# Kernel tuning notes

Hardware: AMD Instinct MI355X
Metric: run time of the kernel (lower is better)

Reference implementation:

```python
import jax, jax.numpy as jnp
import numpy as np

N = 50000      # nodes
E = 1600000    # edges (avg degree 32)
F_IN = 128     # num_features
DIM = 64       # hidden dim
L = 3          # num_gc_layers
G = 500        # graphs in batch


def setup_inputs() -> dict:
    key = jax.random.key(0)
    ks = jax.random.split(key, 16)
    inp = {}
    inp["x"] = jax.random.normal(ks[0], (N, F_IN), dtype=jnp.float32)
    inp["edge_index"] = jax.random.randint(ks[1], (2, E), 0, N, dtype=jnp.int32)
    inp["batch"] = jnp.sort(jax.random.randint(ks[2], (N,), 0, G, dtype=jnp.int32))
    # GIN layer MLP params: layer0 maps F_IN->DIM->DIM, later layers DIM->DIM->DIM
    d_in = F_IN
    ki = 3
    for i in range(L):
        inp[f"W1_{i}"] = jax.random.normal(ks[ki], (d_in, DIM), dtype=jnp.float32) / np.sqrt(d_in); ki += 1
        inp[f"b1_{i}"] = jnp.zeros((DIM,), dtype=jnp.float32)
        inp[f"W2_{i}"] = jax.random.normal(ks[ki], (DIM, DIM), dtype=jnp.float32) / np.sqrt(DIM); ki += 1
        inp[f"b2_{i}"] = jnp.zeros((DIM,), dtype=jnp.float32)
        d_in = DIM
    # final scoring head: concat readout -> dim * L inputs, 1 output
    inp["Wm"] = jax.random.normal(ks[ki], (DIM * L, 1), dtype=jnp.float32) / np.sqrt(DIM * L)
    inp["bm"] = jnp.zeros((1,), dtype=jnp.float32)
    return inp


def _segment_softmax(scores, seg, num_segments):
    # numerically stable softmax over elements grouped by seg; scores [M, 1]
    m = jax.ops.segment_max(scores, seg, num_segments=num_segments)
    e = jnp.exp(scores - m[seg])
    denom = jax.ops.segment_sum(e, seg, num_segments=num_segments)
    return e / denom[seg]


def _forward(x, edge_index, batch, params):
    src, dst = edge_index[0], edge_index[1]
    n = x.shape[0]
    xs = []
    h = x
    for i in range(L):
        W1, b1, W2, b2 = params[4 * i: 4 * i + 4]
        # GINConv (eps=0): h_i <- MLP(h_i + sum_{j->i} h_j)
        agg = jax.ops.segment_sum(h[src], dst, num_segments=n)
        h = jax.nn.relu((h + agg) @ W1 + b1) @ W2 + b2
        if i != L - 1:
            h = jax.nn.relu(h)
        xs.append(h)
    node_prob = jnp.concatenate(xs, axis=1)            # concat readout [N, DIM*L]
    Wm, bm = params[4 * L], params[4 * L + 1]
    node_score = node_prob @ Wm + bm                   # [N, 1]
    # lift_node_score_to_edge_score
    src_score = node_score[src]                        # [E, 1]
    dst_score = node_score[dst]
    edge_score = src_score * dst_score
    edge_prop = _segment_softmax(edge_score, dst, n)   # softmax over edges per dst
    new_score = jax.ops.segment_sum(src_score * edge_prop, dst, num_segments=n)
    node_score = node_score + new_score
    # final softmax over nodes grouped by graph id
    return _segment_softmax(node_score, batch, G)


def reference(x, edge_index, batch, W1_0, b1_0, W2_0, b2_0, W1_1, b1_1, W2_1, b2_1,
              W1_2, b1_2, W2_2, b2_2, Wm, bm):
    params = [W1_0, b1_0, W2_0, b2_0, W1_1, b1_1, W2_1, b2_1,
              W1_2, b1_2, W2_2, b2_2, Wm, bm]
    return _forward(x, edge_index, batch, params)
```

## Files before the change

kernel.cpp:

```cpp
#include <hip/hip_runtime.h>
#include <hip/hip_fp16.h>
#include <math.h>

#define N_NODES 50000
#define N_EDGES 1600000
#define N_GRAPH 500
#define CHUNKS 128
#define EPC (N_EDGES / CHUNKS)
#define NP1 (N_NODES + 1)
#define NIT ((EPC + 1023) / 1024)
#define HALF_N (N_NODES / 2)
#define HNP1 (HALF_N + 1)

__device__ __forceinline__ float rl(float v, int k) {
    return __int_as_float(__builtin_amdgcn_readlane(__float_as_int(v), k));
}
__device__ __forceinline__ void hacc16(float4& A, float4& B, uint4 w) {
    float2 f0 = __half22float2(*reinterpret_cast<__half2*>(&w.x));
    float2 f1 = __half22float2(*reinterpret_cast<__half2*>(&w.y));
    float2 f2 = __half22float2(*reinterpret_cast<__half2*>(&w.z));
    float2 f3 = __half22float2(*reinterpret_cast<__half2*>(&w.w));
    A.x += f0.x; A.y += f0.y; A.z += f1.x; A.w += f1.y;
    B.x += f2.x; B.y += f2.y; B.z += f3.x; B.w += f3.y;
}

__global__ __launch_bounds__(1024) void histsort_kernel(const int* __restrict__ src,
                                                        const int* __restrict__ dst,
                                                        int* __restrict__ csrc_chunk,
                                                        unsigned short* __restrict__ locs) {
    __shared__ unsigned packed[HALF_N / 2];
    __shared__ unsigned aux[1024];
    const int c = blockIdx.x >> 1;
    const int h = blockIdx.x & 1;
    const int lo = h * HALF_N;
    const int s0 = c * EPC;
    const int tid = threadIdx.x;

    for (int i = tid; i < HALF_N / 2; i += 1024) packed[i] = 0;
    __syncthreads();

    unsigned short lrv[NIT];
#pragma unroll
    for (int it = 0; it < NIT; it++) {
        int e = s0 + it * 1024 + tid;
        if (e < s0 + EPC) {
            int d = dst[e];
            int ld = d - lo;
            if (ld >= 0 && ld < HALF_N) {
                int sh = (ld & 1) * 16;
                unsigned old = atomicAdd(&packed[ld >> 1], 1u << sh);
                lrv[it] = (unsigned short)((old >> sh) & 0xffffu);
            }
        }
    }
    __syncthreads();

    const int W = 13;
    int w0 = tid * W;
    int w1 = min(w0 + W, HALF_N / 2);
    unsigned run = 0;
    for (int i = w0; i < w1; i++) {
        unsigned v = packed[i];
        unsigned plo = v & 0xffffu, phi = v >> 16;
        packed[i] = run | ((run + plo) << 16);
        run += plo + phi;
    }
    aux[tid] = run;
    __syncthreads();
    for (int off = 1; off < 1024; off <<= 1) {
        unsigned t = (tid >= off) ? aux[tid - off] : 0;
        __syncthreads();
        aux[tid] += t;
        __syncthreads();
    }
    unsigned b0 = (tid == 0) ? 0 : aux[tid - 1];
    if (b0) {
        unsigned addv = b0 | (b0 << 16);
        for (int i = w0; i < w1; i++) packed[i] += addv;
    }
    __syncthreads();
    unsigned total = aux[1023];

    int* outc = csrc_chunk + (size_t)(c * 2 + h) * EPC;
#pragma unroll
    for (int it = 0; it < NIT; it++) {
        int e = s0 + it * 1024 + tid;
        if (e < s0 + EPC) {
            int d = dst[e];
            int ld = d - lo;
            if (ld >= 0 && ld < HALF_N) {
                unsigned pw = packed[ld >> 1];
                unsigned loc = (ld & 1) ? (pw >> 16) : (pw & 0xffffu);
                outc[loc + lrv[it]] = src[e];
            }
        }
    }
    unsigned short* lc = locs + (size_t)(c * 2 + h) * HNP1;
    for (int ld = tid; ld <= HALF_N; ld += 1024) {
        unsigned short v;
        if (ld == HALF_N) {
            v = (unsigned short)total;
        } else {
            unsigned pw = packed[ld >> 1];
            v = (unsigned short)((ld & 1) ? (pw >> 16) : (pw & 0xffffu));
        }
        lc[ld] = v;
    }
}

__global__ __launch_bounds__(1024) void base_scan1_kernel(const unsigned short* __restrict__ locs,
                                                          unsigned short* __restrict__ base,
                                                          int* __restrict__ deg,
                                                          int* __restrict__ part, int N) {
    int d = blockIdx.x * 1024 + threadIdx.x;
    int run = 0;
    if (d < N) {
        int h = (d >= HALF_N) ? 1 : 0;
        int ld = d - h * HALF_N;
#pragma unroll 8
        for (int c = 0; c < CHUNKS; c++) {
            const unsigned short* lc = locs + (size_t)(c * 2 + h) * HNP1;
            int l0 = lc[ld];
            int l1 = lc[ld + 1];
            base[(size_t)c * N + d] = (unsigned short)run;
            run += l1 - l0;
        }
        deg[d] = run;
    }
    int v = run;
#pragma unroll
    for (int o = 32; o >= 1; o >>= 1) v += __shfl_xor(v, o);
    __shared__ int red[16];
    if ((threadIdx.x & 63) == 0) red[threadIdx.x >> 6] = v;
    __syncthreads();
    if (threadIdx.x == 0) {
        int s = 0;
#pragma unroll
        for (int k = 0; k < 16; k++) s += red[k];
        part[blockIdx.x] = s;
    }
}

__global__ __launch_bounds__(1024) void scan3_kernel(const int* __restrict__ deg,
                                                     const int* __restrict__ part,
                                                     int* __restrict__ rowptr, int N, int nb) {
    __shared__ int blockOff;
    __shared__ int wsum[16];
    int lane = threadIdx.x & 63;
    int w = threadIdx.x >> 6;
    if (threadIdx.x < 64) {
        int pv = (lane < nb && lane < (int)blockIdx.x) ? part[lane] : 0;
#pragma unroll
        for (int o = 32; o >= 1; o >>= 1) pv += __shfl_xor(pv, o);
        if (lane == 0) blockOff = pv;
    }
    int i = blockIdx.x * 1024 + threadIdx.x;
    int v = (i < N) ? deg[i] : 0;
    int inc = v;
#pragma unroll
    for (int o = 1; o < 64; o <<= 1) {
        int t = __shfl_up(inc, o);
        if (lane >= o) inc += t;
    }
    if (lane == 63) wsum[w] = inc;
    __syncthreads();
    if (threadIdx.x < 16) {
        int x = wsum[threadIdx.x];
        int xo = x;
#pragma unroll
        for (int o = 1; o < 16; o <<= 1) {
            int t = __shfl_up(x, o);
            if ((int)threadIdx.x >= o) x += t;
        }
        wsum[threadIdx.x] = x - xo;
    }
    __syncthreads();
    int b = blockOff + wsum[w];
    if (i < N) {
        rowptr[i] = b + inc - v;
        if (i == N - 1) rowptr[N] = b + inc;
    }
}

__global__ __launch_bounds__(256) void gatherfill_kernel(const int* __restrict__ csrc_chunk,
                                                         const unsigned short* __restrict__ locs,
                                                         const unsigned short* __restrict__ base,
                                                         const int* __restrict__ rowptr,
                                                         int* __restrict__ csr_src) {
    const int perXcd = N_NODES / 8;
    int xcd = blockIdx.x & 7;
    int idx = (blockIdx.x >> 3) * 4 + (threadIdx.x >> 6);
    if (idx >= perXcd) return;
    int wid = xcd * perXcd + idx;
    int lane = threadIdx.x & 63;
    int h = (wid >= HALF_N) ? 1 : 0;
    int ld = wid - h * HALF_N;
    int rp = rowptr[wid];
#pragma unroll
    for (int cc = 0; cc < 2; cc++) {
        int c = lane + cc * 64;
        const unsigned short* lc = locs + (size_t)(c * 2 + h) * HNP1;
        int l0 = lc[ld];
        int l1 = lc[ld + 1];
        int cnt = l1 - l0;
        int ob = rp + (int)base[(size_t)c * N_NODES + wid];
        const int* in = csrc_chunk + (size_t)(c * 2 + h) * EPC + l0;
        for (int i = 0; i < cnt; i++) csr_src[ob + i] = in[i];
    }
}

__global__ __launch_bounds__(256, 2) void gemm0_kernel(const float* __restrict__ x,
                                                       const float* __restrict__ W1,
                                                       __half* __restrict__ y0,
                                                       int N, int totalWaves) {
    int lane = threadIdx.x & 63;
    int wid = (blockIdx.x * 256 + threadIdx.x) >> 6;
    float wA[64], wB[64];
#pragma unroll
    for (int k = 0; k < 64; k++) wA[k] = W1[k * 64 + lane];
#pragma unroll
    for (int k = 0; k < 64; k++) wB[k] = W1[(64 + k) * 64 + lane];
    for (int node = wid; node < N; node += totalWaves) {
        float xa = x[(size_t)node * 128 + lane];
        float xb = x[(size_t)node * 128 + 64 + lane];
        float a0 = 0.f, a1 = 0.f, a2 = 0.f, a3 = 0.f;
#pragma unroll
        for (int k = 0; k < 64; k += 4) {
            a0 = fmaf(rl(xa, k + 0), wA[k + 0], a0);
            a1 = fmaf(rl(xa, k + 1), wA[k + 1], a1);
            a2 = fmaf(rl(xa, k + 2), wA[k + 2], a2);
            a3 = fmaf(rl(xa, k + 3), wA[k + 3], a3);
        }
#pragma unroll
        for (int k = 0; k < 64; k += 4) {
            a0 = fmaf(rl(xb, k + 0), wB[k + 0], a0);
            a1 = fmaf(rl(xb, k + 1), wB[k + 1], a1);
            a2 = fmaf(rl(xb, k + 2), wB[k + 2], a2);
            a3 = fmaf(rl(xb, k + 3), wB[k + 3], a3);
        }
        y0[(size_t)node * 64 + lane] = __float2half((a0 + a1) + (a2 + a3));
    }
}

__global__ __launch_bounds__(256) void agg_kernel(const __half* __restrict__ yh,
                                                  const int* __restrict__ rowptr,
                                                  const int* __restrict__ csr_src,
                                                  float* __restrict__ u, int N) {
    int wv = (blockIdx.x * 256 + threadIdx.x) >> 6;
    int half = (threadIdx.x >> 5) & 1;
    int node = wv * 2 + half;
    if (node >= N) return;
    int lane = threadIdx.x & 31;
    int q = lane >> 3;
    int r = lane & 7;
    int start = rowptr[node];
    int end = rowptr[node + 1];
    float4 A = make_float4(0.f, 0.f, 0.f, 0.f);
    float4 B = make_float4(0.f, 0.f, 0.f, 0.f);
    int j = start;
    for (; j + 32 <= end; j += 32) {
        int s0 = csr_src[j + q];
        int s1 = csr_src[j + 4 + q];
        int s2 = csr_src[j + 8 + q];
        int s3 = csr_src[j + 12 + q];
        int s4 = csr_src[j + 16 + q];
        int s5 = csr_src[j + 20 + q];
        int s6 = csr_src[j + 24 + q];
        int s7 = csr_src[j + 28 + q];
        uint4 w0 = *(const uint4*)(yh + (size_t)s0 * 64 + r * 8);
        uint4 w1 = *(const uint4*)(yh + (size_t)s1 * 64 + r * 8);
        uint4 w2 = *(const uint4*)(yh + (size_t)s2 * 64 + r * 8);
        uint4 w3 = *(const uint4*)(yh + (size_t)s3 * 64 + r * 8);
        uint4 w4 = *(const uint4*)(yh + (size_t)s4 * 64 + r * 8);
        uint4 w5 = *(const uint4*)(yh + (size_t)s5 * 64 + r * 8);
        uint4 w6 = *(const uint4*)(yh + (size_t)s6 * 64 + r * 8);
        uint4 w7 = *(const uint4*)(yh + (size_t)s7 * 64 + r * 8);
        hacc16(A, B, w0); hacc16(A, B, w1); hacc16(A, B, w2); hacc16(A, B, w3);
        hacc16(A, B, w4); hacc16(A, B, w5); hacc16(A, B, w6); hacc16(A, B, w7);
    }
#pragma unroll
    for (int m = 0; m < 8; m++) {
        int e = j + 4 * m + q;
        if (e < end) {
            int s = csr_src[e];
            uint4 w = *(const uint4*)(yh + (size_t)s * 64 + r * 8);
            hacc16(A, B, w);
        }
    }
#pragma unroll
    for (int o = 8; o <= 16; o <<= 1) {
        A.x += __shfl_xor(A.x, o); A.y += __shfl_xor(A.y, o);
        A.z += __shfl_xor(A.z, o); A.w += __shfl_xor(A.w, o);
        B.x += __shfl_xor(B.x, o); B.y += __shfl_xor(B.y, o);
        B.z += __shfl_xor(B.z, o); B.w += __shfl_xor(B.w, o);
    }
    if (lane < 8) {
        uint4 w = *(const uint4*)(yh + (size_t)node * 64 + r * 8);
        hacc16(A, B, w);
        *(float4*)(u + (size_t)node * 64 + r * 8) = A;
        *(float4*)(u + (size_t)node * 64 + r * 8 + 4) = B;
    }
}

template <int LAYER>
__global__ __launch_bounds__(256, 2) void mlpAB_kernel(const float* __restrict__ u,
                                                       const float* __restrict__ b1,
                                                       const float* __restrict__ W2,
                                                       const float* __restrict__ b2,
                                                       const float* __restrict__ W1n,
                                                       const float* __restrict__ Wm,
                                                       __half* __restrict__ ynext,
                                                       float* __restrict__ score,
                                                       int N, int totalWaves) {
    int lane = threadIdx.x & 63;
    int wid = (blockIdx.x * 256 + threadIdx.x) >> 6;
    float w2[64], w1[64];
#pragma unroll
    for (int k = 0; k < 64; k++) w2[k] = W2[k * 64 + lane];
#pragma unroll
    for (int k = 0; k < 64; k++) w1[k] = W1n[k * 64 + lane];
    float bb1 = b1[lane], bb2 = b2[lane], wm = Wm[LAYER * 64 + lane];

    int node = wid;
    float uin = (node < N) ? u[(size_t)node * 64 + lane] : 0.f;
    for (; node < N; node += totalWaves) {
        int nn = node + totalWaves;
        float unext = (nn < N) ? u[(size_t)nn * 64 + lane] : 0.f;
        float t = fmaxf(uin + bb1, 0.f);
        float a0 = 0.f, a1 = 0.f, a2 = 0.f, a3 = 0.f;
#pragma unroll
        for (int k = 0; k < 64; k += 4) {
            a0 = fmaf(rl(t, k + 0), w2[k + 0], a0);
            a1 = fmaf(rl(t, k + 1), w2[k + 1], a1);
            a2 = fmaf(rl(t, k + 2), w2[k + 2], a2);
            a3 = fmaf(rl(t, k + 3), w2[k + 3], a3);
        }
        float h = fmaxf(bb2 + ((a0 + a1) + (a2 + a3)), 0.f);
        float p = h * wm;
#pragma unroll
        for (int o = 32; o >= 1; o >>= 1) p += __shfl_xor(p, o);
        if (lane == 0) {
            if (LAYER == 0) score[node] = p;
            else score[node] += p;
        }
        float y0 = 0.f, y1 = 0.f, y2 = 0.f, y3 = 0.f;
#pragma unroll
        for (int k = 0; k < 64; k += 4) {
            y0 = fmaf(rl(h, k + 0), w1[k + 0], y0);
            y1 = fmaf(rl(h, k + 1), w1[k + 1], y1);
            y2 = fmaf(rl(h, k + 2), w1[k + 2], y2);
            y3 = fmaf(rl(h, k + 3), w1[k + 3], y3);
        }
        ynext[(size_t)node * 64 + lane] = __float2half((y0 + y1) + (y2 + y3));
        uin = unext;
    }
}

__global__ __launch_bounds__(256, 2) void mlpA2_kernel(const float* __restrict__ u,
                                                       const float* __restrict__ b1,
                                                       const float* __restrict__ W2,
                                                       const float* __restrict__ b2,
                                                       const float* __restrict__ Wm,
                                                       float* __restrict__ score,
                                                       int N, int totalWaves) {
    int lane = threadIdx.x & 63;
    int wid = (blockIdx.x * 256 + threadIdx.x) >> 6;
    float w2[64];
#pragma unroll
    for (int k = 0; k < 64; k++) w2[k] = W2[k * 64 + lane];
    float bb1 = b1[lane], bb2 = b2[lane], wm = Wm[2 * 64 + lane];

    int node = wid;
    float uin = (node < N) ? u[(size_t)node * 64 + lane] : 0.f;
    for (; node < N; node += totalWaves) {
        int nn = node + totalWaves;
        float unext = (nn < N) ? u[(size_t)nn * 64 + lane] : 0.f;
        float t = fmaxf(uin + bb1, 0.f);
        float a0 = 0.f, a1 = 0.f, a2 = 0.f, a3 = 0.f;
#pragma unroll
        for (int k = 0; k < 64; k += 4) {
            a0 = fmaf(rl(t, k + 0), w2[k + 0], a0);
            a1 = fmaf(rl(t, k + 1), w2[k + 1], a1);
            a2 = fmaf(rl(t, k + 2), w2[k + 2], a2);
            a3 = fmaf(rl(t, k + 3), w2[k + 3], a3);
        }
        float h = bb2 + ((a0 + a1) + (a2 + a3));
        float p = h * wm;
#pragma unroll
        for (int o = 32; o >= 1; o >>= 1) p += __shfl_xor(p, o);
        if (lane == 0) score[node] += p;
        uin = unext;
    }
}

__global__ __launch_bounds__(256) void edge_softmax_kernel(const float* __restrict__ score,
                                                           const int* __restrict__ rowptr,
                                                           const int* __restrict__ csr_src,
                                                           const float* __restrict__ bm,
                                                           float* __restrict__ nsf, int N) {
    int wid = (blockIdx.x * blockDim.x + threadIdx.x) >> 6;
    int lane = threadIdx.x & 63;
    if (wid >= N) return;
    float b = bm[0];
    float sd = score[wid] + b;
    int start = rowptr[wid];
    int end = rowptr[wid + 1];
    bool has0 = (start + lane < end);
    float ss0 = 0.f;
    float m = -INFINITY;
    if (has0) {
        ss0 = score[csr_src[start + lane]] + b;
        m = ss0 * sd;
    }
    for (int j = start + 64 + lane; j < end; j += 64) {
        float ss = score[csr_src[j]] + b;
        m = fmaxf(m, ss * sd);
    }
#pragma unroll
    for (int o = 32; o >= 1; o >>= 1) m = fmaxf(m, __shfl_xor(m, o));
    float se = 0.f, swe = 0.f;
    if (m > -INFINITY) {
        if (has0) {
            float e0 = expf(ss0 * sd - m);
            se += e0;
            swe += ss0 * e0;
        }
        for (int j = start + 64 + lane; j < end; j += 64) {
            float ss = score[csr_src[j]] + b;
            float e = expf(ss * sd - m);
            se += e;
            swe += ss * e;
        }
#pragma unroll
        for (int o = 32; o >= 1; o >>= 1) {
            se += __shfl_xor(se, o);
            swe += __shfl_xor(swe, o);
        }
    }
    float ns = (se > 0.f) ? (swe / se) : 0.f;
    if (lane == 0) nsf[wid] = sd + ns;
}

__global__ __launch_bounds__(256) void graph_softmax_kernel(const float* __restrict__ nsf,
                                                            const int* __restrict__ batch,
                                                            float* __restrict__ out, int N) {
    int g = blockIdx.x;
    int tid = threadIdx.x;
    int lo = 0, hi = N;
    while (lo < hi) { int mid = (lo + hi) >> 1; if (batch[mid] < g) lo = mid + 1; else hi = mid; }
    int s0 = lo;
    hi = N;
    while (lo < hi) { int mid = (lo + hi) >> 1; if (batch[mid] < g + 1) lo = mid + 1; else hi = mid; }
    int s1 = lo;

    __shared__ float red[4];
    __shared__ float bval;
    float m = -INFINITY;
    for (int i = s0 + tid; i < s1; i += 256) m = fmaxf(m, nsf[i]);
#pragma unroll
    for (int o = 32; o >= 1; o >>= 1) m = fmaxf(m, __shfl_xor(m, o));
    if ((tid & 63) == 0) red[tid >> 6] = m;
    __syncthreads();
    if (tid == 0) bval = fmaxf(fmaxf(red[0], red[1]), fmaxf(red[2], red[3]));
    __syncthreads();
    float bmx = bval;
    float s = 0.f;
    for (int i = s0 + tid; i < s1; i += 256) {
        float e = expf(nsf[i] - bmx);
        out[i] = e;
        s += e;
    }
#pragma unroll
    for (int o = 32; o >= 1; o >>= 1) s += __shfl_xor(s, o);
    __syncthreads();
    if ((tid & 63) == 0) red[tid >> 6] = s;
    __syncthreads();
    if (tid == 0) bval = red[0] + red[1] + red[2] + red[3];
    __syncthreads();
    float inv = 1.f / bval;
    for (int i = s0 + tid; i < s1; i += 256) out[i] *= inv;
}

extern "C" void kernel_launch(void* const* d_in, const int* in_sizes, int n_in,
                              void* d_out, int out_size, void* d_ws, size_t ws_size,
                              hipStream_t stream) {
    const int N = N_NODES, E = N_EDGES;

    const float* x = (const float*)d_in[0];
    const int* ei = (const int*)d_in[1];
    const int* batch = (const int*)d_in[2];
    const float* W1a[3] = {(const float*)d_in[3], (const float*)d_in[7], (const float*)d_in[11]};
    const float* b1a[3] = {(const float*)d_in[4], (const float*)d_in[8], (const float*)d_in[12]};
    const float* W2a[3] = {(const float*)d_in[5], (const float*)d_in[9], (const float*)d_in[13]};
    const float* b2a[3] = {(const float*)d_in[6], (const float*)d_in[10], (const float*)d_in[14]};
    const float* Wm = (const float*)d_in[15];
    const float* bm = (const float*)d_in[16];
    float* out = (float*)d_out;

    const int* srcp = ei;
    const int* dstp = ei + E;

    float* ubuf = (float*)d_ws;
    int* csrc_chunk = (int*)ubuf;
    __half* yA = (__half*)(ubuf + (size_t)N * 64);
    __half* yB = yA + (size_t)N * 64;
    float* score = (float*)(yB + (size_t)N * 64);
    float* nsf = score + N;
    int* deg = (int*)(nsf + N);
    int* rowptr = deg + N;
    int* part = rowptr + N + 1;
    int* csr_src = part + 64;
    unsigned short* locs = (unsigned short*)(csr_src + E);
    unsigned short* base = locs + (size_t)2 * CHUNKS * HNP1;

    histsort_kernel<<<CHUNKS * 2, 1024, 0, stream>>>(srcp, dstp, csrc_chunk, locs);

    const int nbScan = (N + 1023) / 1024;
    base_scan1_kernel<<<nbScan, 1024, 0, stream>>>(locs, base, deg, part, N);
    scan3_kernel<<<nbScan, 1024, 0, stream>>>(deg, part, rowptr, N, nbScan);

    const int gfBlocks = 8 * ((N / 8 + 3) / 4);
    gatherfill_kernel<<<gfBlocks, 256, 0, stream>>>(csrc_chunk, locs, base, rowptr, csr_src);

    const int gw = 4096;
    gemm0_kernel<<<1024, 256, 0, stream>>>(x, W1a[0], yA, N, gw);

    int aggBlocks = (N / 2 + 3) / 4;

    agg_kernel<<<aggBlocks, 256, 0, stream>>>(yA, rowptr, csr_src, ubuf, N);
    mlpAB_kernel<0><<<1024, 256, 0, stream>>>(ubuf, b1a[0], W2a[0], b2a[0], W1a[1], Wm, yB, score, N, gw);

    agg_kernel<<<aggBlocks, 256, 0, stream>>>(yB, rowptr, csr_src, ubuf, N);
    mlpAB_kernel<1><<<1024, 256, 0, stream>>>(ubuf, b1a[1], W2a[1], b2a[1], W1a[2], Wm, yA, score, N, gw);

    agg_kernel<<<aggBlocks, 256, 0, stream>>>(yA, rowptr, csr_src, ubuf, N);
    mlpA2_kernel<<<1024, 256, 0, stream>>>(ubuf, b1a[2], W2a[2], b2a[2], Wm, score, N, gw);

    edge_softmax_kernel<<<(N + 3) / 4, 256, 0, stream>>>(score, rowptr, csr_src, bm, nsf, N);

    graph_softmax_kernel<<<N_GRAPH, 256, 0, stream>>>(nsf, batch, out, N);
}
```

Before: 320.5 us.

## Restructure per-node MLP kernels to thread-per-node with LDS transpose and pre-transposed weights

The MLP kernels change from one wavefront per node with readlane broadcasts to one thread per node. Node features are staged through a padded LDS tile and transposed into registers. The weights are pre-transposed by a new small kernel, so each output column is a contiguous row that all threads read uniformly, which should become scalar loads. The aim is to remove the readlane-bound serial inner loop and raise throughput. In exchange it uses heavy register use (v[64]), a 33KB LDS tile per 128-thread block, and one extra kernel launch.

```diff
diff --git a/kernel.cpp b/kernel.cpp
--- a/kernel.cpp
+++ b/kernel.cpp
@@ -11,6 +11,8 @@
 #define NIT ((EPC + 1023) / 1024)
 #define HALF_N (N_NODES / 2)
 #define HNP1 (HALF_N + 1)
+#define MLPB 128
+#define PITCH 129
 
 __device__ __forceinline__ float rl(float v, int k) {
     return __int_as_float(__builtin_amdgcn_readlane(__float_as_int(v), k));
@@ -206,6 +208,19 @@
         int ob = rp + (int)base[(size_t)c * N_NODES + wid];
         const int* in = csrc_chunk + (size_t)(c * 2 + h) * EPC + l0;
         for (int i = 0; i < cnt; i++) csr_src[ob + i] = in[i];
+    }
+}
+
+struct TPtrs {
+    const float* in[5];
+    float* out[5];
+};
+__global__ __launch_bounds__(256) void transpose64_kernel(TPtrs p) {
+    const float* in = p.in[blockIdx.x];
+    float* out = p.out[blockIdx.x];
+    for (int i = threadIdx.x; i < 4096; i += 256) {
+        int o = i >> 6, k = i & 63;
+        out[o * 64 + k] = in[k * 64 + o];
     }
 }
 
@@ -303,94 +318,133 @@
 }
 
 template <int LAYER>
-__global__ __launch_bounds__(256, 2) void mlpAB_kernel(const float* __restrict__ u,
-                                                       const float* __restrict__ b1,
-                                                       const float* __restrict__ W2,
-                                                       const float* __restrict__ b2,
-                                                       const float* __restrict__ W1n,
-                                                       const float* __restrict__ Wm,
-                                                       __half* __restrict__ ynext,
-                                                       float* __restrict__ score,
-                                                       int N, int totalWaves) {
-    int lane = threadIdx.x & 63;
-    int wid = (blockIdx.x * 256 + threadIdx.x) >> 6;
-    float w2[64], w1[64];
-#pragma unroll
-    for (int k = 0; k < 64; k++) w2[k] = W2[k * 64 + lane];
-#pragma unroll
-    for (int k = 0; k < 64; k++) w1[k] = W1n[k * 64 + lane];
-    float bb1 = b1[lane], bb2 = b2[lane], wm = Wm[LAYER * 64 + lane];
-
-    int node = wid;
-    float uin = (node < N) ? u[(size_t)node * 64 + lane] : 0.f;
-    for (; node < N; node += totalWaves) {
-        int nn = node + totalWaves;
-        float unext = (nn < N) ? u[(size_t)nn * 64 + lane] : 0.f;
-        float t = fmaxf(uin + bb1, 0.f);
+__global__ __launch_bounds__(MLPB) void mlpABT_kernel(const float* __restrict__ u,
+                                                      const float* __restrict__ b1,
+                                                      const float* __restrict__ W2T,
+                                                      const float* __restrict__ b2,
+                                                      const float* __restrict__ W1nT,
+                                                      const float* __restrict__ Wm,
+                                                      __half* __restrict__ ynext,
+                                                      float* __restrict__ score, int N) {
+    __shared__ float tile[64 * PITCH];
+    int tid = threadIdx.x;
+    int blockBase = blockIdx.x * MLPB;
+    for (int i = 0; i < 16; i++) {
+        int idx = i * MLPB + tid;
+        int nn = idx >> 4;
+        int f4 = idx & 15;
+        int g = blockBase + nn;
+        float4 v = (g < N) ? *(const float4*)(u + (size_t)g * 64 + f4 * 4)
+                           : make_float4(0.f, 0.f, 0.f, 0.f);
+        tile[(f4 * 4 + 0) * PITCH + nn] = v.x;
+        tile[(f4 * 4 + 1) * PITCH + nn] = v.y;
+        tile[(f4 * 4 + 2) * PITCH + nn] = v.z;
+        tile[(f4 * 4 + 3) * PITCH + nn] = v.w;
+    }
+    __syncthreads();
+    float v[64];
+#pragma unroll
+    for (int k = 0; k < 64; k++) v[k] = fmaxf(tile[k * PITCH + tid] + b1[k], 0.f);
+    __syncthreads();
+#pragma unroll 2
+    for (int o = 0; o < 64; o++) {
+        const float* wc = W2T + o * 64;
         float a0 = 0.f, a1 = 0.f, a2 = 0.f, a3 = 0.f;
 #pragma unroll
         for (int k = 0; k < 64; k += 4) {
-            a0 = fmaf(rl(t, k + 0), w2[k + 0], a0);
-            a1 = fmaf(rl(t, k + 1), w2[k + 1], a1);
-            a2 = fmaf(rl(t, k + 2), w2[k + 2], a2);
-            a3 = fmaf(rl(t, k + 3), w2[k + 3], a3);
-        }
-        float h = fmaxf(bb2 + ((a0 + a1) + (a2 + a3)), 0.f);
-        float p = h * wm;
-#pragma unroll
-        for (int o = 32; o >= 1; o >>= 1) p += __shfl_xor(p, o);
-        if (lane == 0) {
-            if (LAYER == 0) score[node] = p;
-            else score[node] += p;
-        }
-        float y0 = 0.f, y1 = 0.f, y2 = 0.f, y3 = 0.f;
+            a0 = fmaf(v[k + 0], wc[k + 0], a0);
+            a1 = fmaf(v[k + 1], wc[k + 1], a1);
+            a2 = fmaf(v[k + 2], wc[k + 2], a2);
+            a3 = fmaf(v[k + 3], wc[k + 3], a3);
+        }
+        tile[o * PITCH + tid] = fmaxf(b2[o] + ((a0 + a1) + (a2 + a3)), 0.f);
+    }
+#pragma unroll
+    for (int k = 0; k < 64; k++) v[k] = tile[k * PITCH + tid];
+    float p = 0.f;
+#pragma unroll
+    for (int k = 0; k < 64; k++) p = fmaf(v[k], Wm[LAYER * 64 + k], p);
+    int gn = blockBase + tid;
+    if (gn < N) {
+        if (LAYER == 0) score[gn] = p;
+        else score[gn] += p;
+    }
+#pragma unroll 2
+    for (int o = 0; o < 64; o++) {
+        const float* wc = W1nT + o * 64;
+        float a0 = 0.f, a1 = 0.f, a2 = 0.f, a3 = 0.f;
 #pragma unroll
         for (int k = 0; k < 64; k += 4) {
-            y0 = fmaf(rl(h, k + 0), w1[k + 0], y0);
-            y1 = fmaf(rl(h, k + 1), w1[k + 1], y1);
-            y2 = fmaf(rl(h, k + 2), w1[k + 2], y2);
-            y3 = fmaf(rl(h, k + 3), w1[k + 3], y3);
-        }
-        ynext[(size_t)node * 64 + lane] = __float2half((y0 + y1) + (y2 + y3));
-        uin = unext;
-    }
-}
-
-__global__ __launch_bounds__(256, 2) void mlpA2_kernel(const float* __restrict__ u,
-                                                       const float* __restrict__ b1,
-                                                       const float* __restrict__ W2,
-                                                       const float* __restrict__ b2,
-                                                       const float* __restrict__ Wm,
-                                                       float* __restrict__ score,
-                                                       int N, int totalWaves) {
-    int lane = threadIdx.x & 63;
-    int wid = (blockIdx.x * 256 + threadIdx.x) >> 6;
-    float w2[64];
-#pragma unroll
-    for (int k = 0; k < 64; k++) w2[k] = W2[k * 64 + lane];
-    float bb1 = b1[lane], bb2 = b2[lane], wm = Wm[2 * 64 + lane];
-
-    int node = wid;
-    float uin = (node < N) ? u[(size_t)node * 64 + lane] : 0.f;
-    for (; node < N; node += totalWaves) {
-        int nn = node + totalWaves;
-        float unext = (nn < N) ? u[(size_t)nn * 64 + lane] : 0.f;
-        float t = fmaxf(uin + bb1, 0.f);
+            a0 = fmaf(v[k + 0], wc[k + 0], a0);
+            a1 = fmaf(v[k + 1], wc[k + 1], a1);
+            a2 = fmaf(v[k + 2], wc[k + 2], a2);
+            a3 = fmaf(v[k + 3], wc[k + 3], a3);
+        }
+        tile[o * PITCH + tid] = (a0 + a1) + (a2 + a3);
+    }
+    __syncthreads();
+    for (int i = 0; i < 16; i++) {
+        int idx = i * MLPB + tid;
+        int nn = idx >> 4;
+        int f4 = idx & 15;
+        int g = blockBase + nn;
+        if (g < N) {
+            float x0 = tile[(f4 * 4 + 0) * PITCH + nn];
+            float x1 = tile[(f4 * 4 + 1) * PITCH + nn];
+            float x2 = tile[(f4 * 4 + 2) * PITCH + nn];
+            float x3 = tile[(f4 * 4 + 3) * PITCH + nn];
+            __half2 p01 = __halves2half2(__float2half(x0), __float2half(x1));
+            __half2 p23 = __halves2half2(__float2half(x2), __float2half(x3));
+            uint2 pk;
+            pk.x = *reinterpret_cast<unsigned*>(&p01);
+            pk.y = *reinterpret_cast<unsigned*>(&p23);
+            *(uint2*)(ynext + (size_t)g * 64 + f4 * 4) = pk;
+        }
+    }
+}
+
+__global__ __launch_bounds__(MLPB) void mlpA2T_kernel(const float* __restrict__ u,
+                                                      const float* __restrict__ b1,
+                                                      const float* __restrict__ W2T,
+                                                      const float* __restrict__ b2,
+                                                      const float* __restrict__ Wm,
+                                                      float* __restrict__ score, int N) {
+    __shared__ float tile[64 * PITCH];
+    int tid = threadIdx.x;
+    int blockBase = blockIdx.x * MLPB;
+    for (int i = 0; i < 16; i++) {
+        int idx = i * MLPB + tid;
+        int nn = idx >> 4;
+        int f4 = idx & 15;
+        int g = blockBase + nn;
+        float4 v = (g < N) ? *(const float4*)(u + (size_t)g * 64 + f4 * 4)
+                           : make_float4(0.f, 0.f, 0.f, 0.f);
+        tile[(f4 * 4 + 0) * PITCH + nn] = v.x;
+        tile[(f4 * 4 + 1) * PITCH + nn] = v.y;
+        tile[(f4 * 4 + 2) * PITCH + nn] = v.z;
+        tile[(f4 * 4 + 3) * PITCH + nn] = v.w;
+    }
+    __syncthreads();
+    float v[64];
+#pragma unroll
+    for (int k = 0; k < 64; k++) v[k] = fmaxf(tile[k * PITCH + tid] + b1[k], 0.f);
+    float p = 0.f;
+#pragma unroll 2
+    for (int o = 0; o < 64; o++) {
+        const float* wc = W2T + o * 64;
         float a0 = 0.f, a1 = 0.f, a2 = 0.f, a3 = 0.f;
 #pragma unroll
         for (int k = 0; k < 64; k += 4) {
-            a0 = fmaf(rl(t, k + 0), w2[k + 0], a0);
-            a1 = fmaf(rl(t, k + 1), w2[k + 1], a1);
-            a2 = fmaf(rl(t, k + 2), w2[k + 2], a2);
-            a3 = fmaf(rl(t, k + 3), w2[k + 3], a3);
-        }
-        float h = bb2 + ((a0 + a1) + (a2 + a3));
-        float p = h * wm;
-#pragma unroll
-        for (int o = 32; o >= 1; o >>= 1) p += __shfl_xor(p, o);
-        if (lane == 0) score[node] += p;
-        uin = unext;
-    }
+            a0 = fmaf(v[k + 0], wc[k + 0], a0);
+            a1 = fmaf(v[k + 1], wc[k + 1], a1);
+            a2 = fmaf(v[k + 2], wc[k + 2], a2);
+            a3 = fmaf(v[k + 3], wc[k + 3], a3);
+        }
+        float h = b2[o] + ((a0 + a1) + (a2 + a3));
+        p = fmaf(h, Wm[2 * 64 + o], p);
+    }
+    int gn = blockBase + tid;
+    if (gn < N) score[gn] += p;
 }
 
 __global__ __launch_bounds__(256) void edge_softmax_kernel(const float* __restrict__ score,
@@ -512,6 +566,15 @@
     int* csr_src = part + 64;
     unsigned short* locs = (unsigned short*)(csr_src + E);
     unsigned short* base = locs + (size_t)2 * CHUNKS * HNP1;
+    float* wt = (float*)(base + (size_t)CHUNKS * N);
+
+    TPtrs tp;
+    tp.in[0] = W2a[0]; tp.out[0] = wt + 0 * 4096;
+    tp.in[1] = W2a[1]; tp.out[1] = wt + 1 * 4096;
+    tp.in[2] = W2a[2]; tp.out[2] = wt + 2 * 4096;
+    tp.in[3] = W1a[1]; tp.out[3] = wt + 3 * 4096;
+    tp.in[4] = W1a[2]; tp.out[4] = wt + 4 * 4096;
+    transpose64_kernel<<<5, 256, 0, stream>>>(tp);
 
     histsort_kernel<<<CHUNKS * 2, 1024, 0, stream>>>(srcp, dstp, csrc_chunk, locs);
 
@@ -526,15 +589,19 @@
     gemm0_kernel<<<1024, 256, 0, stream>>>(x, W1a[0], yA, N, gw);
 
     int aggBlocks = (N / 2 + 3) / 4;
+    int mlpBlocks = (N + MLPB - 1) / MLPB;
 
     agg_kernel<<<aggBlocks, 256, 0, stream>>>(yA, rowptr, csr_src, ubuf, N);
-    mlpAB_kernel<0><<<1024, 256, 0, stream>>>(ubuf, b1a[0], W2a[0], b2a[0], W1a[1], Wm, yB, score, N, gw);
+    mlpABT_kernel<0><<<mlpBlocks, MLPB, 0, stream>>>(ubuf, b1a[0], wt + 0 * 4096, b2a[0],
+                                                     wt + 3 * 4096, Wm, yB, score, N);
 
     agg_kernel<<<aggBlocks, 256, 0, stream>>>(yB, rowptr, csr_src, ubuf, N);
-    mlpAB_kernel<1><<<1024, 256, 0, stream>>>(ubuf, b1a[1], W2a[1], b2a[1], W1a[2], Wm, yA, score, N, gw);
+    mlpABT_kernel<1><<<mlpBlocks, MLPB, 0, stream>>>(ubuf, b1a[1], wt + 1 * 4096, b2a[1],
+                                                     wt + 4 * 4096, Wm, yA, score, N);
 
     agg_kernel<<<aggBlocks, 256, 0, stream>>>(yA, rowptr, csr_src, ubuf, N);
-    mlpA2_kernel<<<1024, 256, 0, stream>>>(ubuf, b1a[2], W2a[2], b2a[2], Wm, score, N, gw);
+    mlpA2T_kernel<<<mlpBlocks, MLPB, 0, stream>>>(ubuf, b1a[2], wt + 2 * 4096, b2a[2],
+                                                  Wm, score, N);
 
     edge_softmax_kernel<<<(N + 3) / 4, 256, 0, stream>>>(score, rowptr, csr_src, bm, nsf, N);
 
```

Result: slower. 482.9 us (median of 3 runs) (+50.7%).
